# Optimization experiments

Hardware: AMD Instinct MI355X
Metric: run time of the kernel (lower is better)

The kernel has to match this reference:

```python
import jax, jax.numpy as jnp
import numpy as np

B, T, D, H = 4, 4096, 128, 4
DH = D // H
FF = 2 * D
EPS = 1e-5


def _layernorm(x, g, b):
    mu = jnp.mean(x, axis=-1, keepdims=True)
    var = jnp.mean(jnp.square(x - mu), axis=-1, keepdims=True)
    return (x - mu) * jax.lax.rsqrt(var + EPS) * g + b


def setup_inputs() -> dict:
    key = jax.random.key(0)
    ks = jax.random.split(key, 12)

    def lin(k, fan_in, shape):
        return (jax.random.normal(k, shape, jnp.float32) / np.sqrt(fan_in)).astype(jnp.float32)

    return {
        "x": jax.random.normal(ks[0], (B, T, D), jnp.float32),
        "adj_mask": jax.random.randint(ks[1], (T, T), 0, 2).astype(bool),
        # weights stored (in, out); apply as x @ W + b
        "Wq": lin(ks[2], D, (D, D)), "bq": jnp.zeros((D,), jnp.float32),
        "Wk": lin(ks[3], D, (D, D)), "bk": jnp.zeros((D,), jnp.float32),
        "Wv": lin(ks[4], D, (D, D)), "bv": jnp.zeros((D,), jnp.float32),
        "Wo": lin(ks[5], D, (D, D)), "bo": jnp.zeros((D,), jnp.float32),
        "ln1_g": jnp.ones((D,), jnp.float32), "ln1_b": jnp.zeros((D,), jnp.float32),
        "W1": lin(ks[6], D, (D, FF)), "b1": jnp.zeros((FF,), jnp.float32),
        "W2": lin(ks[7], FF, (FF, D)), "b2": jnp.zeros((D,), jnp.float32),
        "ln2_g": jnp.ones((D,), jnp.float32), "ln2_b": jnp.zeros((D,), jnp.float32),
    }


def reference(x, adj_mask, Wq, bq, Wk, bk, Wv, bv, Wo, bo,
              ln1_g, ln1_b, W1, b1, W2, b2, ln2_g, ln2_b):
    b, t, d = x.shape
    q = (x @ Wq + bq).reshape(b, t, H, DH)
    k = (x @ Wk + bk).reshape(b, t, H, DH)
    v = (x @ Wv + bv).reshape(b, t, H, DH)

    # scores: (b, h, t, t)
    scores = jnp.einsum('bihd,bjhd->bhij', q, k) / np.sqrt(DH).astype(np.float32)
    full_mask = adj_mask | jnp.eye(t, dtype=bool)          # (t, t)
    scores = jnp.where(full_mask[None, None], scores, -jnp.inf)
    attn = jax.nn.softmax(scores, axis=-1)
    attn = jnp.where(jnp.isnan(attn), 0.0, attn)           # NaN cleanup as in source

    out = jnp.einsum('bhij,bjhd->bihd', attn, v).reshape(b, t, d)
    out = out @ Wo + bo
    x = _layernorm(x + out, ln1_g, ln1_b)
    ff = jax.nn.gelu(x @ W1 + b1, approximate=False) @ W2 + b2
    return _layernorm(x + ff, ln2_g, ln2_b)
```

## Files before the change

kernel.cpp:

```cpp
#include <hip/hip_runtime.h>
#include <hip/hip_bf16.h>
#include <math.h>


#define B_ 4
#define T_ 4096
#define D_ 128
#define H_ 4
#define DH_ 32
#define FF_ 256
#define M_ (B_*T_)

typedef unsigned short u16;
typedef __attribute__((ext_vector_type(8))) short bf16x8;
typedef __attribute__((ext_vector_type(4))) float f32x4;
typedef __attribute__((ext_vector_type(4))) u16 u16x4;

constexpr size_t OFF_FLAG  = 0;
constexpr size_t OFF_MASKW = 256;
constexpr size_t OFF_XB    = OFF_MASKW + 2097152;
constexpr size_t OFF_WQKVT = OFF_XB    + 4194304;
constexpr size_t OFF_WOT   = OFF_WQKVT + 98304;
constexpr size_t OFF_W1T   = OFF_WOT   + 32768;
constexpr size_t OFF_W2T   = OFF_W1T   + 65536;
constexpr size_t OFF_QW    = OFF_W2T   + 65536;
constexpr size_t OFF_KW    = OFF_QW    + 4194304;
constexpr size_t OFF_VT    = OFF_KW    + 4194304;
constexpr size_t OFF_AO    = OFF_VT    + 4194304;

__device__ __forceinline__ u16 f2bf(float f){
  unsigned u = __float_as_uint(f);
  u += 0x7FFFu + ((u >> 16) & 1u);
  return (u16)(u >> 16);
}

__device__ __forceinline__ float bf2f(u16 b){
  return __uint_as_float((unsigned)b << 16);
}

__device__ __forceinline__ bf16x8 load_frag(const u16* p){
  union { bf16x8 v; uint2 u[2]; } f;
  f.u[0] = *(const uint2*)(p);
  f.u[1] = *(const uint2*)(p + 16);
  return f.v;
}

__global__ void k_detect(const unsigned* m, unsigned* flags){
  const int i = blockIdx.x*256 + threadIdx.x;
  const unsigned w = m[i];
  const int li = (w <= 1u);
  const int lf = (w == 0u || w == 0x3F800000u);
  if (!__all(li)){ if ((threadIdx.x & 63) == 0) atomicAnd(&flags[0], 0u); }
  if (!__all(lf)){ if ((threadIdx.x & 63) == 0) atomicAnd(&flags[1], 0u); }
}

__global__ void k_pack(const void* mask, const unsigned* flags, unsigned* mw){
  int idx = blockIdx.x*256 + threadIdx.x;
  int i = idx >> 7, wj = idx & 127;
  unsigned w = 0;
  if (flags[0] | flags[1]){
    const uint4* p = (const uint4*)((const unsigned*)mask + (size_t)i*T_ + wj*32);
    #pragma unroll
    for (int j = 0; j < 8; j++){
      uint4 v = p[j];
      w |= (unsigned)(v.x != 0u) << (4*j);
      w |= (unsigned)(v.y != 0u) << (4*j + 1);
      w |= (unsigned)(v.z != 0u) << (4*j + 2);
      w |= (unsigned)(v.w != 0u) << (4*j + 3);
    }
  } else {
    const uint4* p = (const uint4*)((const unsigned char*)mask + (size_t)i*T_ + wj*32);
    uint4 A = p[0], B = p[1];
    #define NIB_(d) ((((d) & 0x01010101u) * 0x01020408u) >> 24)
    w  =  NIB_(A.x)        | (NIB_(A.y) << 4)  | (NIB_(A.z) << 8)  | (NIB_(A.w) << 12)
       | (NIB_(B.x) << 16) | (NIB_(B.y) << 20) | (NIB_(B.z) << 24) | (NIB_(B.w) << 28);
    #undef NIB_
  }
  if ((i >> 5) == wj) w |= 1u << (i & 31);
  mw[idx] = w;
}

__global__ void k_conv_w(const float* Wq, const float* Wk, const float* Wv, const float* Wo,
                         const float* W1, const float* W2,
                         u16* wqkvt, u16* wot, u16* w1t, u16* w2t){
  int idx = blockIdx.x*256 + threadIdx.x;
  if (idx < 49152){
    int n = idx >> 7, k = idx & 127;
    float v = (n < 128) ? Wq[k*128 + n] : (n < 256 ? Wk[k*128 + (n-128)] : Wv[k*128 + (n-256)]);
    wqkvt[idx] = f2bf(v);
  } else if (idx < 65536){
    int j = idx - 49152, n = j >> 7, k = j & 127;
    wot[j] = f2bf(Wo[k*128 + n]);
  } else if (idx < 98304){
    int j = idx - 65536, n = j >> 7, k = j & 127;
    w1t[j] = f2bf(W1[k*256 + n]);
  } else if (idx < 131072){
    int j = idx - 98304, n = j >> 8, k = j & 255;
    w2t[j] = f2bf(W2[k*128 + n]);
  }
}

__global__ __launch_bounds__(256) void k_qkv(const float* x, const u16* wt,
    const float* bq, const float* bk, const float* bv,
    u16* qw, u16* kw, u16* vt, float* kmax2){
  __shared__ u16 xt[16][136];
  __shared__ u16 st[16][392];
  const int wv = threadIdx.x >> 6, lane = threadIdx.x & 63;
  const int r15 = lane & 15, g = lane >> 4;
  const int m0 = blockIdx.x * 16;
  {
    const int row = threadIdx.x >> 4, c0 = (threadIdx.x & 15) * 8;
    const float* xp = x + (size_t)(m0 + row)*D_ + c0;
    float4 a = *(const float4*)(xp);
    float4 b = *(const float4*)(xp + 4);
    u16x4 o1 = { f2bf(a.x), f2bf(a.y), f2bf(a.z), f2bf(a.w) };
    u16x4 o2 = { f2bf(b.x), f2bf(b.y), f2bf(b.z), f2bf(b.w) };
    *(u16x4*)&xt[row][c0]     = o1;
    *(u16x4*)&xt[row][c0 + 4] = o2;
  }
  __syncthreads();
  f32x4 acc[6] = {};
  #pragma unroll
  for (int kk = 0; kk < D_; kk += 32){
    bf16x8 af = load_frag(&xt[r15][kk + 4*g]);
    #pragma unroll
    for (int nf = 0; nf < 6; nf++){
      const u16* br = wt + (size_t)(wv*96 + nf*16 + r15)*D_ + kk + 4*g;
      acc[nf] = __builtin_amdgcn_mfma_f32_16x16x32_bf16(af, load_frag(br), acc[nf], 0, 0, 0);
    }
  }
  #pragma unroll
  for (int nf = 0; nf < 6; nf++){
    int ncol = wv*96 + nf*16 + r15;
    float bias = (ncol < 128) ? bq[ncol] : (ncol < 256 ? bk[ncol-128] : bv[ncol-256]);
    float scl  = (ncol < 128) ? 0.17677669529663687f : 1.f;
    #pragma unroll
    for (int rr = 0; rr < 4; rr++)
      st[4*g + rr][ncol] = f2bf((acc[nf][rr] + bias) * scl);
  }
  __syncthreads();
  const int b = m0 >> 12, t0m = m0 & (T_-1);
  const int i = threadIdx.x;
  {
    const int t = i >> 4, c = i & 15, h = c >> 2, d0 = (c & 3)*8;
    uint4 v = *(const uint4*)&st[t][h*32 + d0];
    *(uint4*)(qw + ((size_t)(b*H_ + h)*T_ + (t0m + t))*DH_ + d0) = v;
  }
  {
    const int h = i >> 6, seg = (i >> 4) & 3, trow = i & 15;
    union { u16 e[8]; uint4 u; } v;
    #pragma unroll
    for (int sub = 0; sub < 8; sub++){
      int d = 16*(sub >> 2) + 4*seg + (sub & 3);
      v.e[sub] = st[trow][128 + h*32 + d];
    }
    *(uint4*)(kw + (size_t)(b*H_ + h)*T_*DH_ + (size_t)(t0m >> 4)*512 + seg*128 + trow*8) = v.u;
  }
  {
    const int bit4 = (t0m >> 4) & 1;
    #pragma unroll
    for (int cc = 0; cc < 2; cc++){
      const int c = i + cc*256;
      const int h = c >> 7, dlhi = (c >> 6) & 1, tq = (c >> 4) & 3, dl15 = c & 15;
      u16x4 v;
      #pragma unroll
      for (int j = 0; j < 4; j++)
        v[j] = st[tq*4 + j][256 + h*32 + dlhi*16 + dl15];
      *(u16x4*)(vt + (size_t)(b*H_ + h)*T_*DH_ + (size_t)(t0m >> 5)*1024
                + dlhi*512 + (size_t)(tq*16 + dl15)*8 + 4*bit4) = v;
    }
  }
  if (i < 64){
    const int t = i >> 2, h = i & 3;
    float s = 0.f;
    #pragma unroll
    for (int d = 0; d < 32; d++){ float f = bf2f(st[t][128 + h*32 + d]); s += f*f; }
    #pragma unroll
    for (int d = 4; d < 64; d <<= 1) s = fmaxf(s, __shfl_xor(s, d));
    if (i < 4) atomicMax((unsigned*)(kmax2 + (b*H_ + h)), __float_as_uint(s));
  }
}

__global__ __launch_bounds__(256, 4) void k_attn16(const u16* qw, const u16* kw, const u16* vt,
    const unsigned* mw, const float* kmax2, u16* ao){
  const int wg = (blockIdx.x & 7)*128 + (blockIdx.x >> 3);
  const int wv = threadIdx.x >> 6, lane = threadIdx.x & 63;
  const int r15 = lane & 15, g = lane >> 4;
  const int bh = wg >> 6;
  const int q0 = (wg & 63)*64 + wv*16;
  const u16* qp = qw + (size_t)bh*T_*DH_;
  const u16* kl = kw + (size_t)bh*T_*DH_ + lane*8;
  const u16* vl = vt + (size_t)bh*T_*DH_ + lane*8;
  const unsigned* mrow = mw + (size_t)(q0 + r15)*(T_/32);
  const bf16x8 qf = load_frag(qp + (size_t)(q0 + r15)*DH_ + 4*g);
  float n0 = 0.f;
  #pragma unroll
  for (int j = 0; j < 8; j++){ float f = bf2f((u16)qf[j]); n0 += f*f; }
  n0 += __shfl_xor(n0, 16); n0 += __shfl_xor(n0, 32);
  const float bnd = sqrtf(n0 * kmax2[bh]) * 1.0001f + 1e-6f;
  union { u16 e[8]; bf16x8 v; } ones;
  #pragma unroll
  for (int j = 0; j < 8; j++) ones.e[j] = 0x3F80;
  f32x4 o0 = {}, o1 = {}, ol = {};
  for (int jb4 = 0; jb4 < T_; jb4 += 128){
    const uint4 wv4 = *(const uint4*)(mrow + (jb4 >> 5));
    #pragma unroll
    for (int ji = 0; ji < 4; ji++){
      const int jb = jb4 + ji*32;
      const unsigned w = ((const unsigned*)&wv4)[ji];
      const unsigned u = w >> (4*g);
      bf16x8 kf0 = *(const bf16x8*)(kl + (size_t)(jb >> 4)*512);
      bf16x8 kf1 = *(const bf16x8*)(kl + (size_t)((jb >> 4) + 1)*512);
      bf16x8 vf0 = *(const bf16x8*)(vl + (size_t)(jb >> 5)*1024);
      bf16x8 vf1 = *(const bf16x8*)(vl + (size_t)(jb >> 5)*1024 + 512);
      f32x4 c0, c1;
      #pragma unroll
      for (int rr = 0; rr < 4; rr++){
        c0[rr] = ((u >> rr) & 1u)        ? -bnd : -1e30f;
        c1[rr] = ((u >> (16 + rr)) & 1u) ? -bnd : -1e30f;
      }
      f32x4 s0 = __builtin_amdgcn_mfma_f32_16x16x32_bf16(kf0, qf, c0, 0, 0, 0);
      f32x4 s1 = __builtin_amdgcn_mfma_f32_16x16x32_bf16(kf1, qf, c1, 0, 0, 0);
      float p0[4], p1[4];
      #pragma unroll
      for (int rr = 0; rr < 4; rr++){
        p0[rr] = __expf(s0[rr]);
        p1[rr] = __expf(s1[rr]);
      }
      union { bf16x8 v; __hip_bfloat162 h2[4]; } pf;
      pf.h2[0] = __float22bfloat162_rn(make_float2(p0[0], p0[1]));
      pf.h2[1] = __float22bfloat162_rn(make_float2(p0[2], p0[3]));
      pf.h2[2] = __float22bfloat162_rn(make_float2(p1[0], p1[1]));
      pf.h2[3] = __float22bfloat162_rn(make_float2(p1[2], p1[3]));
      o0 = __builtin_amdgcn_mfma_f32_16x16x32_bf16(pf.v, vf0, o0, 0, 0, 0);
      o1 = __builtin_amdgcn_mfma_f32_16x16x32_bf16(pf.v, vf1, o1, 0, 0, 0);
      ol = __builtin_amdgcn_mfma_f32_16x16x32_bf16(pf.v, ones.v, ol, 0, 0, 0);
    }
  }
  const int b = bh >> 2, h = bh & 3;
  #pragma unroll
  for (int rr = 0; rr < 4; rr++){
    float li = ol[rr];
    float inv = li > 0.f ? 1.f/li : 0.f;
    size_t row = (size_t)(b*T_ + q0 + 4*g + rr)*D_;
    ao[row + h*DH_ + r15]      = f2bf(o0[rr]*inv);
    ao[row + h*DH_ + 16 + r15] = f2bf(o1[rr]*inv);
  }
}

__global__ __launch_bounds__(256) void k_tail(const u16* ao, const u16* wot, const float* bo,
    const float* x, const float* g1, const float* be1,
    const u16* w1t, const float* bf1, const u16* w2t, const float* b2,
    const float* g2, const float* be2, float* out){
  __shared__ float ly[16][132];
  __shared__ u16  lyb[16][136];
  __shared__ u16  lhb[16][264];
  __shared__ float rs[4][16], rq[4][16];
  const int wv = threadIdx.x >> 6, lane = threadIdx.x & 63;
  const int r15 = lane & 15, g = lane >> 4;
  const int m0 = blockIdx.x * 16;

  f32x4 accA[2] = {};
  const u16* ar = ao + (size_t)(m0 + r15)*D_ + 4*g;
  #pragma unroll
  for (int kk = 0; kk < D_; kk += 32){
    bf16x8 af = load_frag(ar + kk);
    #pragma unroll
    for (int nf = 0; nf < 2; nf++)
      accA[nf] = __builtin_amdgcn_mfma_f32_16x16x32_bf16(af,
          load_frag(wot + (size_t)((wv*2 + nf)*16 + r15)*D_ + kk + 4*g), accA[nf], 0, 0, 0);
  }
  float tA[2][4];
  #pragma unroll
  for (int rr = 0; rr < 4; rr++){
    float s1 = 0.f, s2 = 0.f;
    #pragma unroll
    for (int nf = 0; nf < 2; nf++){
      int col = (wv*2 + nf)*16 + r15;
      float t = accA[nf][rr] + bo[col] + x[(size_t)(m0 + 4*g + rr)*D_ + col];
      tA[nf][rr] = t; s1 += t; s2 += t*t;
    }
    #pragma unroll
    for (int d = 1; d < 16; d <<= 1){ s1 += __shfl_xor(s1, d); s2 += __shfl_xor(s2, d); }
    if (r15 == 0){ rs[wv][4*g + rr] = s1; rq[wv][4*g + rr] = s2; }
  }
  __syncthreads();
  #pragma unroll
  for (int rr = 0; rr < 4; rr++){
    int row = 4*g + rr;
    float S1 = rs[0][row] + rs[1][row] + rs[2][row] + rs[3][row];
    float S2 = rq[0][row] + rq[1][row] + rq[2][row] + rq[3][row];
    float mu = S1 * (1.f/D_);
    float var = fmaxf(S2 * (1.f/D_) - mu*mu, 0.f);
    float inv = rsqrtf(var + 1e-5f);
    #pragma unroll
    for (int nf = 0; nf < 2; nf++){
      int col = (wv*2 + nf)*16 + r15;
      float o = (tA[nf][rr] - mu)*inv*g1[col] + be1[col];
      ly[row][col] = o;
      lyb[row][col] = f2bf(o);
    }
  }
  __syncthreads();

  const int n0w = wv*64;
  f32x4 accB[4] = {};
  #pragma unroll
  for (int kk = 0; kk < D_; kk += 32){
    bf16x8 af = load_frag(&lyb[r15][kk + 4*g]);
    #pragma unroll
    for (int nf = 0; nf < 4; nf++)
      accB[nf] = __builtin_amdgcn_mfma_f32_16x16x32_bf16(af,
          load_frag(w1t + (size_t)(n0w + nf*16 + r15)*D_ + kk + 4*g), accB[nf], 0, 0, 0);
  }
  #pragma unroll
  for (int nf = 0; nf < 4; nf++){
    int col = n0w + nf*16 + r15;
    float bias = bf1[col];
    #pragma unroll
    for (int rr = 0; rr < 4; rr++){
      float vv = accB[nf][rr] + bias;
      float z2 = fminf(1.5957691216057308f*vv + 0.07135581778225507f*vv*vv*vv, 80.f);
      float t = __expf(z2);
      lhb[4*g + rr][col] = f2bf(vv * t / (t + 1.f));
    }
  }
  __syncthreads();

  f32x4 accC[2] = {};
  #pragma unroll
  for (int kk = 0; kk < FF_; kk += 32){
    bf16x8 af = load_frag(&lhb[r15][kk + 4*g]);
    #pragma unroll
    for (int nf = 0; nf < 2; nf++)
      accC[nf] = __builtin_amdgcn_mfma_f32_16x16x32_bf16(af,
          load_frag(w2t + (size_t)((wv*2 + nf)*16 + r15)*FF_ + kk + 4*g), accC[nf], 0, 0, 0);
  }
  float tC[2][4];
  #pragma unroll
  for (int rr = 0; rr < 4; rr++){
    float s1 = 0.f, s2 = 0.f;
    #pragma unroll
    for (int nf = 0; nf < 2; nf++){
      int col = (wv*2 + nf)*16 + r15;
      float t = accC[nf][rr] + b2[col] + ly[4*g + rr][col];
      tC[nf][rr] = t; s1 += t; s2 += t*t;
    }
    #pragma unroll
    for (int d = 1; d < 16; d <<= 1){ s1 += __shfl_xor(s1, d); s2 += __shfl_xor(s2, d); }
    if (r15 == 0){ rs[wv][4*g + rr] = s1; rq[wv][4*g + rr] = s2; }
  }
  __syncthreads();
  #pragma unroll
  for (int rr = 0; rr < 4; rr++){
    int row = 4*g + rr;
    float S1 = rs[0][row] + rs[1][row] + rs[2][row] + rs[3][row];
    float S2 = rq[0][row] + rq[1][row] + rq[2][row] + rq[3][row];
    float mu = S1 * (1.f/D_);
    float var = fmaxf(S2 * (1.f/D_) - mu*mu, 0.f);
    float inv = rsqrtf(var + 1e-5f);
    #pragma unroll
    for (int nf = 0; nf < 2; nf++){
      int col = (wv*2 + nf)*16 + r15;
      out[(size_t)(m0 + row)*D_ + col] = (tC[nf][rr] - mu)*inv*g2[col] + be2[col];
    }
  }
}

extern "C" void kernel_launch(void* const* d_in, const int* in_sizes, int n_in,
                              void* d_out, int out_size, void* d_ws, size_t ws_size,
                              hipStream_t stream){
  const float* x   = (const float*)d_in[0];
  const void*  msk = d_in[1];
  const float* Wq = (const float*)d_in[2];  const float* bq  = (const float*)d_in[3];
  const float* Wk = (const float*)d_in[4];  const float* bk  = (const float*)d_in[5];
  const float* Wv = (const float*)d_in[6];  const float* bv  = (const float*)d_in[7];
  const float* Wo = (const float*)d_in[8];  const float* bo  = (const float*)d_in[9];
  const float* g1 = (const float*)d_in[10]; const float* be1 = (const float*)d_in[11];
  const float* W1 = (const float*)d_in[12]; const float* bf1 = (const float*)d_in[13];
  const float* W2 = (const float*)d_in[14]; const float* b2  = (const float*)d_in[15];
  const float* g2 = (const float*)d_in[16]; const float* be2 = (const float*)d_in[17];

  char* ws = (char*)d_ws;
  unsigned* flags = (unsigned*)(ws + OFF_FLAG);
  float*    kmax2 = (float*)   (ws + OFF_FLAG + 64);
  unsigned* mw    = (unsigned*)(ws + OFF_MASKW);
  u16* wqkvt = (u16*)(ws + OFF_WQKVT);
  u16* wot   = (u16*)(ws + OFF_WOT);
  u16* w1t   = (u16*)(ws + OFF_W1T);
  u16* w2t   = (u16*)(ws + OFF_W2T);
  u16* qw    = (u16*)(ws + OFF_QW);
  u16* kw    = (u16*)(ws + OFF_KW);
  u16* vt    = (u16*)(ws + OFF_VT);
  u16* ao    = (u16*)(ws + OFF_AO);

  hipMemsetAsync(ws + OFF_FLAG, 1, 8, stream);
  hipMemsetAsync(ws + OFF_FLAG + 64, 0, 64, stream);
  k_detect<<<64, 256, 0, stream>>>((const unsigned*)msk, flags);
  k_pack  <<<(T_*T_/32)/256, 256, 0, stream>>>(msk, flags, mw);
  k_conv_w<<<131072/256, 256, 0, stream>>>(Wq, Wk, Wv, Wo, W1, W2, wqkvt, wot, w1t, w2t);
  k_qkv   <<<M_/16, 256, 0, stream>>>(x, wqkvt, bq, bk, bv, qw, kw, vt, kmax2);
  k_attn16<<<(B_*H_)*(T_/64), 256, 0, stream>>>(qw, kw, vt, mw, kmax2, ao);
  k_tail  <<<M_/16, 256, 0, stream>>>(ao, wot, bo, x, g1, be1, w1t, bf1, w2t, b2, g2, be2, (float*)d_out);
}
```

Before: 188.0 us.

## Merge prep kernels, fold kmax2 memset into detect, double tail rows per block

Merges the mask-packing and weight-conversion kernels into one launch and moves the kmax2 zeroing into k_detect, dropping a memset. This removes two launches and their gaps. k_tail now processes 32 rows per block instead of 16, so each weight fragment feeds two MFMAs and half as many blocks are launched. In exchange k_tail uses more registers and shared memory, which may lower occupancy.

```diff
diff --git a/kernel.cpp b/kernel.cpp
--- a/kernel.cpp
+++ b/kernel.cpp
@@ -45,7 +45,8 @@
   return f.v;
 }
 
-__global__ void k_detect(const unsigned* m, unsigned* flags){
+__global__ void k_detect(const unsigned* m, unsigned* flags, float* kmax2){
+  if (blockIdx.x == 0 && threadIdx.x < 16) kmax2[threadIdx.x] = 0.f;
   const int i = blockIdx.x*256 + threadIdx.x;
   const unsigned w = m[i];
   const int li = (w <= 1u);
@@ -54,49 +55,50 @@
   if (!__all(lf)){ if ((threadIdx.x & 63) == 0) atomicAnd(&flags[1], 0u); }
 }
 
-__global__ void k_pack(const void* mask, const unsigned* flags, unsigned* mw){
-  int idx = blockIdx.x*256 + threadIdx.x;
-  int i = idx >> 7, wj = idx & 127;
-  unsigned w = 0;
-  if (flags[0] | flags[1]){
-    const uint4* p = (const uint4*)((const unsigned*)mask + (size_t)i*T_ + wj*32);
-    #pragma unroll
-    for (int j = 0; j < 8; j++){
-      uint4 v = p[j];
-      w |= (unsigned)(v.x != 0u) << (4*j);
-      w |= (unsigned)(v.y != 0u) << (4*j + 1);
-      w |= (unsigned)(v.z != 0u) << (4*j + 2);
-      w |= (unsigned)(v.w != 0u) << (4*j + 3);
-    }
+__global__ void k_prep(const void* mask, const unsigned* flags, unsigned* mw,
+                       const float* Wq, const float* Wk, const float* Wv, const float* Wo,
+                       const float* W1, const float* W2,
+                       u16* wqkvt, u16* wot, u16* w1t, u16* w2t){
+  if (blockIdx.x < 2048){
+    int idx = blockIdx.x*256 + threadIdx.x;
+    int i = idx >> 7, wj = idx & 127;
+    unsigned w = 0;
+    if (flags[0] | flags[1]){
+      const uint4* p = (const uint4*)((const unsigned*)mask + (size_t)i*T_ + wj*32);
+      #pragma unroll
+      for (int j = 0; j < 8; j++){
+        uint4 v = p[j];
+        w |= (unsigned)(v.x != 0u) << (4*j);
+        w |= (unsigned)(v.y != 0u) << (4*j + 1);
+        w |= (unsigned)(v.z != 0u) << (4*j + 2);
+        w |= (unsigned)(v.w != 0u) << (4*j + 3);
+      }
+    } else {
+      const uint4* p = (const uint4*)((const unsigned char*)mask + (size_t)i*T_ + wj*32);
+      uint4 A = p[0], B = p[1];
+      #define NIB_(d) ((((d) & 0x01010101u) * 0x01020408u) >> 24)
+      w  =  NIB_(A.x)        | (NIB_(A.y) << 4)  | (NIB_(A.z) << 8)  | (NIB_(A.w) << 12)
+         | (NIB_(B.x) << 16) | (NIB_(B.y) << 20) | (NIB_(B.z) << 24) | (NIB_(B.w) << 28);
+      #undef NIB_
+    }
+    if ((i >> 5) == wj) w |= 1u << (i & 31);
+    mw[idx] = w;
   } else {
-    const uint4* p = (const uint4*)((const unsigned char*)mask + (size_t)i*T_ + wj*32);
-    uint4 A = p[0], B = p[1];
-    #define NIB_(d) ((((d) & 0x01010101u) * 0x01020408u) >> 24)
-    w  =  NIB_(A.x)        | (NIB_(A.y) << 4)  | (NIB_(A.z) << 8)  | (NIB_(A.w) << 12)
-       | (NIB_(B.x) << 16) | (NIB_(B.y) << 20) | (NIB_(B.z) << 24) | (NIB_(B.w) << 28);
-    #undef NIB_
-  }
-  if ((i >> 5) == wj) w |= 1u << (i & 31);
-  mw[idx] = w;
-}
-
-__global__ void k_conv_w(const float* Wq, const float* Wk, const float* Wv, const float* Wo,
-                         const float* W1, const float* W2,
-                         u16* wqkvt, u16* wot, u16* w1t, u16* w2t){
-  int idx = blockIdx.x*256 + threadIdx.x;
-  if (idx < 49152){
-    int n = idx >> 7, k = idx & 127;
-    float v = (n < 128) ? Wq[k*128 + n] : (n < 256 ? Wk[k*128 + (n-128)] : Wv[k*128 + (n-256)]);
-    wqkvt[idx] = f2bf(v);
-  } else if (idx < 65536){
-    int j = idx - 49152, n = j >> 7, k = j & 127;
-    wot[j] = f2bf(Wo[k*128 + n]);
-  } else if (idx < 98304){
-    int j = idx - 65536, n = j >> 7, k = j & 127;
-    w1t[j] = f2bf(W1[k*256 + n]);
-  } else if (idx < 131072){
-    int j = idx - 98304, n = j >> 8, k = j & 255;
-    w2t[j] = f2bf(W2[k*128 + n]);
+    int idx = (blockIdx.x - 2048)*256 + threadIdx.x;
+    if (idx < 49152){
+      int n = idx >> 7, k = idx & 127;
+      float v = (n < 128) ? Wq[k*128 + n] : (n < 256 ? Wk[k*128 + (n-128)] : Wv[k*128 + (n-256)]);
+      wqkvt[idx] = f2bf(v);
+    } else if (idx < 65536){
+      int j = idx - 49152, n = j >> 7, k = j & 127;
+      wot[j] = f2bf(Wo[k*128 + n]);
+    } else if (idx < 98304){
+      int j = idx - 65536, n = j >> 7, k = j & 127;
+      w1t[j] = f2bf(W1[k*256 + n]);
+    } else if (idx < 131072){
+      int j = idx - 98304, n = j >> 8, k = j & 255;
+      w2t[j] = f2bf(W2[k*128 + n]);
+    }
   }
 }
 
@@ -181,7 +183,7 @@
   }
 }
 
-__global__ __launch_bounds__(256, 4) void k_attn16(const u16* qw, const u16* kw, const u16* vt,
+__global__ __launch_bounds__(256, 4) void k_attn17(const u16* qw, const u16* kw, const u16* vt,
     const unsigned* mw, const float* kmax2, u16* ao){
   const int wg = (blockIdx.x & 7)*128 + (blockIdx.x >> 3);
   const int wv = threadIdx.x >> 6, lane = threadIdx.x & 63;
@@ -252,117 +254,140 @@
     const float* x, const float* g1, const float* be1,
     const u16* w1t, const float* bf1, const u16* w2t, const float* b2,
     const float* g2, const float* be2, float* out){
-  __shared__ float ly[16][132];
-  __shared__ u16  lyb[16][136];
-  __shared__ u16  lhb[16][264];
-  __shared__ float rs[4][16], rq[4][16];
+  __shared__ float ly[32][132];
+  __shared__ u16  lyb[32][136];
+  __shared__ u16  lhb[32][264];
+  __shared__ float rs[4][32], rq[4][32];
   const int wv = threadIdx.x >> 6, lane = threadIdx.x & 63;
   const int r15 = lane & 15, g = lane >> 4;
-  const int m0 = blockIdx.x * 16;
-
-  f32x4 accA[2] = {};
-  const u16* ar = ao + (size_t)(m0 + r15)*D_ + 4*g;
+  const int m0 = blockIdx.x * 32;
+
+  f32x4 accA[2][2] = {};
   #pragma unroll
   for (int kk = 0; kk < D_; kk += 32){
-    bf16x8 af = load_frag(ar + kk);
-    #pragma unroll
-    for (int nf = 0; nf < 2; nf++)
-      accA[nf] = __builtin_amdgcn_mfma_f32_16x16x32_bf16(af,
-          load_frag(wot + (size_t)((wv*2 + nf)*16 + r15)*D_ + kk + 4*g), accA[nf], 0, 0, 0);
-  }
-  float tA[2][4];
-  #pragma unroll
-  for (int rr = 0; rr < 4; rr++){
-    float s1 = 0.f, s2 = 0.f;
+    bf16x8 af0 = load_frag(ao + (size_t)(m0 + r15)*D_ + kk + 4*g);
+    bf16x8 af1 = load_frag(ao + (size_t)(m0 + 16 + r15)*D_ + kk + 4*g);
     #pragma unroll
     for (int nf = 0; nf < 2; nf++){
-      int col = (wv*2 + nf)*16 + r15;
-      float t = accA[nf][rr] + bo[col] + x[(size_t)(m0 + 4*g + rr)*D_ + col];
-      tA[nf][rr] = t; s1 += t; s2 += t*t;
-    }
-    #pragma unroll
-    for (int d = 1; d < 16; d <<= 1){ s1 += __shfl_xor(s1, d); s2 += __shfl_xor(s2, d); }
-    if (r15 == 0){ rs[wv][4*g + rr] = s1; rq[wv][4*g + rr] = s2; }
-  }
-  __syncthreads();
-  #pragma unroll
-  for (int rr = 0; rr < 4; rr++){
-    int row = 4*g + rr;
-    float S1 = rs[0][row] + rs[1][row] + rs[2][row] + rs[3][row];
-    float S2 = rq[0][row] + rq[1][row] + rq[2][row] + rq[3][row];
-    float mu = S1 * (1.f/D_);
-    float var = fmaxf(S2 * (1.f/D_) - mu*mu, 0.f);
-    float inv = rsqrtf(var + 1e-5f);
+      bf16x8 bf = load_frag(wot + (size_t)((wv*2 + nf)*16 + r15)*D_ + kk + 4*g);
+      accA[0][nf] = __builtin_amdgcn_mfma_f32_16x16x32_bf16(af0, bf, accA[0][nf], 0, 0, 0);
+      accA[1][nf] = __builtin_amdgcn_mfma_f32_16x16x32_bf16(af1, bf, accA[1][nf], 0, 0, 0);
+    }
+  }
+  float tA[2][2][4];
+  #pragma unroll
+  for (int t = 0; t < 2; t++){
+    #pragma unroll
+    for (int rr = 0; rr < 4; rr++){
+      float s1 = 0.f, s2 = 0.f;
+      #pragma unroll
+      for (int nf = 0; nf < 2; nf++){
+        int col = (wv*2 + nf)*16 + r15;
+        float v = accA[t][nf][rr] + bo[col] + x[(size_t)(m0 + t*16 + 4*g + rr)*D_ + col];
+        tA[t][nf][rr] = v; s1 += v; s2 += v*v;
+      }
+      #pragma unroll
+      for (int d = 1; d < 16; d <<= 1){ s1 += __shfl_xor(s1, d); s2 += __shfl_xor(s2, d); }
+      if (r15 == 0){ rs[wv][t*16 + 4*g + rr] = s1; rq[wv][t*16 + 4*g + rr] = s2; }
+    }
+  }
+  __syncthreads();
+  #pragma unroll
+  for (int t = 0; t < 2; t++){
+    #pragma unroll
+    for (int rr = 0; rr < 4; rr++){
+      int row = t*16 + 4*g + rr;
+      float S1 = rs[0][row] + rs[1][row] + rs[2][row] + rs[3][row];
+      float S2 = rq[0][row] + rq[1][row] + rq[2][row] + rq[3][row];
+      float mu = S1 * (1.f/D_);
+      float var = fmaxf(S2 * (1.f/D_) - mu*mu, 0.f);
+      float inv = rsqrtf(var + 1e-5f);
+      #pragma unroll
+      for (int nf = 0; nf < 2; nf++){
+        int col = (wv*2 + nf)*16 + r15;
+        float o = (tA[t][nf][rr] - mu)*inv*g1[col] + be1[col];
+        ly[row][col] = o;
+        lyb[row][col] = f2bf(o);
+      }
+    }
+  }
+  __syncthreads();
+
+  const int n0w = wv*64;
+  f32x4 accB[2][4] = {};
+  #pragma unroll
+  for (int kk = 0; kk < D_; kk += 32){
+    bf16x8 af0 = load_frag(&lyb[r15][kk + 4*g]);
+    bf16x8 af1 = load_frag(&lyb[16 + r15][kk + 4*g]);
+    #pragma unroll
+    for (int nf = 0; nf < 4; nf++){
+      bf16x8 bf = load_frag(w1t + (size_t)(n0w + nf*16 + r15)*D_ + kk + 4*g);
+      accB[0][nf] = __builtin_amdgcn_mfma_f32_16x16x32_bf16(af0, bf, accB[0][nf], 0, 0, 0);
+      accB[1][nf] = __builtin_amdgcn_mfma_f32_16x16x32_bf16(af1, bf, accB[1][nf], 0, 0, 0);
+    }
+  }
+  #pragma unroll
+  for (int t = 0; t < 2; t++){
+    #pragma unroll
+    for (int nf = 0; nf < 4; nf++){
+      int col = n0w + nf*16 + r15;
+      float bias = bf1[col];
+      #pragma unroll
+      for (int rr = 0; rr < 4; rr++){
+        float vv = accB[t][nf][rr] + bias;
+        float z2 = fminf(1.5957691216057308f*vv + 0.07135581778225507f*vv*vv*vv, 80.f);
+        float e = __expf(z2);
+        lhb[t*16 + 4*g + rr][col] = f2bf(vv * e / (e + 1.f));
+      }
+    }
+  }
+  __syncthreads();
+
+  f32x4 accC[2][2] = {};
+  #pragma unroll
+  for (int kk = 0; kk < FF_; kk += 32){
+    bf16x8 af0 = load_frag(&lhb[r15][kk + 4*g]);
+    bf16x8 af1 = load_frag(&lhb[16 + r15][kk + 4*g]);
     #pragma unroll
     for (int nf = 0; nf < 2; nf++){
-      int col = (wv*2 + nf)*16 + r15;
-      float o = (tA[nf][rr] - mu)*inv*g1[col] + be1[col];
-      ly[row][col] = o;
-      lyb[row][col] = f2bf(o);
-    }
-  }
-  __syncthreads();
-
-  const int n0w = wv*64;
-  f32x4 accB[4] = {};
-  #pragma unroll
-  for (int kk = 0; kk < D_; kk += 32){
-    bf16x8 af = load_frag(&lyb[r15][kk + 4*g]);
-    #pragma unroll
-    for (int nf = 0; nf < 4; nf++)
-      accB[nf] = __builtin_amdgcn_mfma_f32_16x16x32_bf16(af,
-          load_frag(w1t + (size_t)(n0w + nf*16 + r15)*D_ + kk + 4*g), accB[nf], 0, 0, 0);
-  }
-  #pragma unroll
-  for (int nf = 0; nf < 4; nf++){
-    int col = n0w + nf*16 + r15;
-    float bias = bf1[col];
+      bf16x8 bf = load_frag(w2t + (size_t)((wv*2 + nf)*16 + r15)*FF_ + kk + 4*g);
+      accC[0][nf] = __builtin_amdgcn_mfma_f32_16x16x32_bf16(af0, bf, accC[0][nf], 0, 0, 0);
+      accC[1][nf] = __builtin_amdgcn_mfma_f32_16x16x32_bf16(af1, bf, accC[1][nf], 0, 0, 0);
+    }
+  }
+  float tC[2][2][4];
+  #pragma unroll
+  for (int t = 0; t < 2; t++){
     #pragma unroll
     for (int rr = 0; rr < 4; rr++){
-      float vv = accB[nf][rr] + bias;
-      float z2 = fminf(1.5957691216057308f*vv + 0.07135581778225507f*vv*vv*vv, 80.f);
-      float t = __expf(z2);
-      lhb[4*g + rr][col] = f2bf(vv * t / (t + 1.f));
-    }
-  }
-  __syncthreads();
-
-  f32x4 accC[2] = {};
-  #pragma unroll
-  for (int kk = 0; kk < FF_; kk += 32){
-    bf16x8 af = load_frag(&lhb[r15][kk + 4*g]);
-    #pragma unroll
-    for (int nf = 0; nf < 2; nf++)
-      accC[nf] = __builtin_amdgcn_mfma_f32_16x16x32_bf16(af,
-          load_frag(w2t + (size_t)((wv*2 + nf)*16 + r15)*FF_ + kk + 4*g), accC[nf], 0, 0, 0);
-  }
-  float tC[2][4];
-  #pragma unroll
-  for (int rr = 0; rr < 4; rr++){
-    float s1 = 0.f, s2 = 0.f;
-    #pragma unroll
-    for (int nf = 0; nf < 2; nf++){
-      int col = (wv*2 + nf)*16 + r15;
-      float t = accC[nf][rr] + b2[col] + ly[4*g + rr][col];
-      tC[nf][rr] = t; s1 += t; s2 += t*t;
-    }
-    #pragma unroll
-    for (int d = 1; d < 16; d <<= 1){ s1 += __shfl_xor(s1, d); s2 += __shfl_xor(s2, d); }
-    if (r15 == 0){ rs[wv][4*g + rr] = s1; rq[wv][4*g + rr] = s2; }
-  }
-  __syncthreads();
-  #pragma unroll
-  for (int rr = 0; rr < 4; rr++){
-    int row = 4*g + rr;
-    float S1 = rs[0][row] + rs[1][row] + rs[2][row] + rs[3][row];
-    float S2 = rq[0][row] + rq[1][row] + rq[2][row] + rq[3][row];
-    float mu = S1 * (1.f/D_);
-    float var = fmaxf(S2 * (1.f/D_) - mu*mu, 0.f);
-    float inv = rsqrtf(var + 1e-5f);
-    #pragma unroll
-    for (int nf = 0; nf < 2; nf++){
-      int col = (wv*2 + nf)*16 + r15;
-      out[(size_t)(m0 + row)*D_ + col] = (tC[nf][rr] - mu)*inv*g2[col] + be2[col];
+      float s1 = 0.f, s2 = 0.f;
+      #pragma unroll
+      for (int nf = 0; nf < 2; nf++){
+        int col = (wv*2 + nf)*16 + r15;
+        float v = accC[t][nf][rr] + b2[col] + ly[t*16 + 4*g + rr][col];
+        tC[t][nf][rr] = v; s1 += v; s2 += v*v;
+      }
+      #pragma unroll
+      for (int d = 1; d < 16; d <<= 1){ s1 += __shfl_xor(s1, d); s2 += __shfl_xor(s2, d); }
+      if (r15 == 0){ rs[wv][t*16 + 4*g + rr] = s1; rq[wv][t*16 + 4*g + rr] = s2; }
+    }
+  }
+  __syncthreads();
+  #pragma unroll
+  for (int t = 0; t < 2; t++){
+    #pragma unroll
+    for (int rr = 0; rr < 4; rr++){
+      int row = t*16 + 4*g + rr;
+      float S1 = rs[0][row] + rs[1][row] + rs[2][row] + rs[3][row];
+      float S2 = rq[0][row] + rq[1][row] + rq[2][row] + rq[3][row];
+      float mu = S1 * (1.f/D_);
+      float var = fmaxf(S2 * (1.f/D_) - mu*mu, 0.f);
+      float inv = rsqrtf(var + 1e-5f);
+      #pragma unroll
+      for (int nf = 0; nf < 2; nf++){
+        int col = (wv*2 + nf)*16 + r15;
+        out[(size_t)(m0 + row)*D_ + col] = (tC[t][nf][rr] - mu)*inv*g2[col] + be2[col];
+      }
     }
   }
 }
@@ -395,11 +420,10 @@
   u16* ao    = (u16*)(ws + OFF_AO);
 
   hipMemsetAsync(ws + OFF_FLAG, 1, 8, stream);
-  hipMemsetAsync(ws + OFF_FLAG + 64, 0, 64, stream);
-  k_detect<<<64, 256, 0, stream>>>((const unsigned*)msk, flags);
-  k_pack  <<<(T_*T_/32)/256, 256, 0, stream>>>(msk, flags, mw);
-  k_conv_w<<<131072/256, 256, 0, stream>>>(Wq, Wk, Wv, Wo, W1, W2, wqkvt, wot, w1t, w2t);
+  k_detect<<<64, 256, 0, stream>>>((const unsigned*)msk, flags, kmax2);
+  k_prep  <<<2560, 256, 0, stream>>>(msk, flags, mw, Wq, Wk, Wv, Wo, W1, W2,
+                                     wqkvt, wot, w1t, w2t);
   k_qkv   <<<M_/16, 256, 0, stream>>>(x, wqkvt, bq, bk, bv, qw, kw, vt, kmax2);
-  k_attn16<<<(B_*H_)*(T_/64), 256, 0, stream>>>(qw, kw, vt, mw, kmax2, ao);
-  k_tail  <<<M_/16, 256, 0, stream>>>(ao, wot, bo, x, g1, be1, w1t, bf1, w2t, b2, g2, be2, (float*)d_out);
-}
+  k_attn17<<<(B_*H_)*(T_/64), 256, 0, stream>>>(qw, kw, vt, mw, kmax2, ao);
+  k_tail  <<<M_/32, 256, 0, stream>>>(ao, wot, bo, x, g1, be1, w1t, bf1, w2t, b2, g2, be2, (float*)d_out);
+}
```

Result: faster. 170.0 us (-9.6%).
